# Kernel optimization log

Hardware: AMD Instinct MI355X
Metric: run time of the kernel (lower is better)

## Reference

```python
import jax, jax.numpy as jnp
import numpy as np

NX, NY = 2, 4          # Cpab tess_size [2, 4]
NT = 4 * NX * NY       # 4 triangles per cell = 32
NSTEPS = 50            # libcpab default numeric integration steps


def _build_tess():
    corner, verts = {}, []
    for j in range(NY + 1):
        for i in range(NX + 1):
            corner[(i, j)] = len(verts); verts.append((i / NX, j / NY))
    center = {}
    for j in range(NY):
        for i in range(NX):
            center[(i, j)] = len(verts); verts.append(((i + 0.5) / NX, (j + 0.5) / NY))
    verts = np.array(verts, np.float64)
    # zero_boundary=True: only interior grid corners + cell centers carry free velocity
    free = [corner[(i, j)] for j in range(1, NY) for i in range(1, NX)]
    free += [center[(i, j)] for j in range(NY) for i in range(NX)]
    tri_vidx = np.zeros((NT, 3), np.int32)
    invP = np.zeros((NT, 3, 3), np.float64)
    for j in range(NY):
        for i in range(NX):
            ll, lr = corner[(i, j)], corner[(i + 1, j)]
            ur, ul = corner[(i + 1, j + 1)], corner[(i, j + 1)]
            c = center[(i, j)]
            for k, tv in enumerate([(ll, lr, c), (lr, ur, c), (ur, ul, c), (ul, ll, c)]):
                t = 4 * (i + j * NX) + k
                tri_vidx[t] = tv
                P = np.vstack([verts[list(tv)].T, np.ones(3)])  # columns [p; 1]
                invP[t] = np.linalg.inv(P)
    return np.array(free, np.int32), tri_vidx, invP.astype(np.float32), len(verts)

FREE_IDX, TRI_VIDX, INVP, NV = _build_tess()
THETA_DIM = 2 * len(FREE_IDX)  # 22


def _findcell(p):
    # p: (..., 2) in [0,1]^2 -> flat triangle index in [0, NT)
    x = jnp.clip(p[..., 0], 0.0, 1.0) * NX
    y = jnp.clip(p[..., 1], 0.0, 1.0) * NY
    cx = jnp.clip(jnp.floor(x), 0, NX - 1)
    cy = jnp.clip(jnp.floor(y), 0, NY - 1)
    xr, yr = x - cx, y - cy
    below_diag = yr <= xr
    below_anti = yr <= 1.0 - xr
    tri = jnp.where(below_diag, jnp.where(below_anti, 0, 1),
                    jnp.where(below_anti, 3, 2))
    return (4 * (cx + cy * NX)).astype(jnp.int32) + tri


def _cpab_transform_grid(theta, H, W):
    # theta (B, 22) -> per-triangle affine maps A (B, NT, 2, 3), then Euler-integrate
    B = theta.shape[0]
    vv = jnp.zeros((B, NV, 2), theta.dtype).at[:, FREE_IDX].set(theta.reshape(B, -1, 2))
    V = vv[:, TRI_VIDX]                                            # (B,NT,3,2) vertex velocities
    A = jnp.einsum('btvc,tvw->btcw', V, jnp.asarray(INVP, theta.dtype))  # (B,NT,2,3)
    gx, gy = jnp.meshgrid(jnp.linspace(0.0, 1.0, W), jnp.linspace(0.0, 1.0, H))
    p0 = jnp.broadcast_to(jnp.stack([gx.ravel(), gy.ravel()], -1), (B, H * W, 2))
    dt = 1.0 / NSTEPS
    bidx = jnp.arange(B)[:, None]

    def step(p, _):
        Ai = A[bidx, _findcell(p)]                                 # (B,HW,2,3)
        v = Ai[..., 0] * p[..., :1] + Ai[..., 1] * p[..., 1:2] + Ai[..., 2]
        return p + dt * v, None

    p, _ = jax.lax.scan(step, p0, None, length=NSTEPS)
    return p                                                       # (B,HW,2)


def _bilinear(data, grid, H, W):
    # data (B,C,H,W), grid (B,HW,2) in [0,1]; clamp-to-border bilinear sampling
    B, C = data.shape[0], data.shape[1]
    gx = jnp.clip(grid[..., 0], 0.0, 1.0) * (W - 1)
    gy = jnp.clip(grid[..., 1], 0.0, 1.0) * (H - 1)
    x0 = jnp.clip(jnp.floor(gx).astype(jnp.int32), 0, W - 2)
    y0 = jnp.clip(jnp.floor(gy).astype(jnp.int32), 0, H - 2)
    wx, wy = gx - x0, gy - y0
    df = data.reshape(B, C, H * W)
    take = jax.vmap(lambda d, l: d[:, l])                          # per-batch gather

    def g(ix, iy):
        return take(df, iy * W + ix)                               # (B,C,HW)

    wx_, wy_ = wx[:, None, :], wy[:, None, :]
    out = (g(x0, y0) * (1 - wx_) * (1 - wy_)
           + g(x0 + 1, y0) * wx_ * (1 - wy_)
           + g(x0, y0 + 1) * (1 - wx_) * wy_
           + g(x0 + 1, y0 + 1) * wx_ * wy_)
    return out.reshape(B, C, H, W)


def setup_inputs() -> dict:
    key = jax.random.key(0)
    k1, k2 = jax.random.split(key)
    x = jax.random.normal(k1, (8, 256, 256, 64), dtype=jnp.float32)
    theta = jax.random.normal(k2, (8, THETA_DIM), dtype=jnp.float32)
    return {"x": x, "theta": theta}


def reference(x, theta):
    B, H, W, C = x.shape
    data = jnp.transpose(x, (0, 3, 1, 2))          # NHWC -> NCHW
    grid_t = _cpab_transform_grid(theta, H, W)     # integrate CPA velocity field
    out = _bilinear(data, grid_t, H, W)            # warp via bilinear sampling
    return jnp.transpose(out, (0, 2, 3, 1))        # NCHW -> NHWC
```

## Files before the change

kernel.cpp:

```cpp
#include <hip/hip_runtime.h>

#define NBATCH 8
#define HH 256
#define WW 256
#define CC 64
#define HWPTS 65536
#define NSTEPS_ 50

typedef float vf4 __attribute__((ext_vector_type(4)));

__global__ __launch_bounds__(256) void cpab_build_A(const float* __restrict__ theta,
                                                    float* __restrict__ Aout) {
  int tid = threadIdx.x;
  int b = tid >> 5, t = tid & 31;
  int cell = t >> 2, k = t & 3;
  int ci = cell & 1, cj = cell >> 1;
  int ll = cj * 3 + ci;
  int lr = ll + 1, ul = ll + 3, ur = ll + 4;
  int cen = 15 + cj * 2 + ci;
  int v0, v1, v2 = cen;
  if (k == 0)      { v0 = ll; v1 = lr; }
  else if (k == 1) { v0 = lr; v1 = ur; }
  else if (k == 2) { v0 = ur; v1 = ul; }
  else             { v0 = ul; v1 = ll; }

  int vs[3] = {v0, v1, v2};
  double xs[3], ys[3];
  float Vx[3], Vy[3];
  for (int q = 0; q < 3; ++q) {
    int v = vs[q];
    if (v < 15) { xs[q] = (double)(v % 3) * 0.5; ys[q] = (double)(v / 3) * 0.25; }
    else { int u = v - 15; xs[q] = ((double)(u & 1) + 0.5) * 0.5;
           ys[q] = ((double)(u >> 1) + 0.5) * 0.25; }
    int s = (v == 4) ? 0 : (v == 7) ? 1 : (v == 10) ? 2 : (v >= 15) ? (v - 12) : -1;
    if (s >= 0) { Vx[q] = theta[b * 22 + 2 * s]; Vy[q] = theta[b * 22 + 2 * s + 1]; }
    else        { Vx[q] = 0.f; Vy[q] = 0.f; }
  }
  double x0 = xs[0], x1 = xs[1], x2 = xs[2];
  double y0 = ys[0], y1 = ys[1], y2 = ys[2];
  double det = x0 * (y1 - y2) - x1 * (y0 - y2) + x2 * (y0 - y1);
  double inv[3][3] = {
      {y1 - y2, x2 - x1, x1 * y2 - x2 * y1},
      {y2 - y0, x0 - x2, x2 * y0 - x0 * y2},
      {y0 - y1, x1 - x0, x0 * y1 - x1 * y0}};
  for (int w = 0; w < 3; ++w) {
    float i0 = (float)(inv[0][w] / det);
    float i1 = (float)(inv[1][w] / det);
    float i2 = (float)(inv[2][w] / det);
    float ax = __fadd_rn(__fadd_rn(__fmul_rn(Vx[0], i0), __fmul_rn(Vx[1], i1)),
                         __fmul_rn(Vx[2], i2));
    float ay = __fadd_rn(__fadd_rn(__fmul_rn(Vy[0], i0), __fmul_rn(Vy[1], i1)),
                         __fmul_rn(Vy[2], i2));
    Aout[b * 192 + (w * 32 + t) * 2]     = ax;
    Aout[b * 192 + (w * 32 + t) * 2 + 1] = ay;
  }
}

__global__ __launch_bounds__(256, 8) void cpab_warp_sample(const float* __restrict__ xin,
                                                           const float* __restrict__ Ain,
                                                           float* __restrict__ out) {
  __shared__ float2 sA2[96];
  __shared__ int    sOff[256];
  __shared__ float4 sW[256];

  int tid = threadIdx.x;
  int bid = blockIdx.x;
  int b = bid & 7;
  int row = bid >> 3;
  int base_hw = row << 8;

  if (tid < 192) ((float*)sA2)[tid] = Ain[b * 192 + tid];
  __syncthreads();

  {
    float px = (tid == 255) ? 1.0f : __fmul_rn((float)tid, 1.0f / 255.0f);
    float py = (row == 255) ? 1.0f : __fmul_rn((float)row, 1.0f / 255.0f);
#pragma unroll 1
    for (int s = 0; s < NSTEPS_; ++s) {
      float xc = fminf(fmaxf(px, 0.f), 1.f) * 2.0f;
      float yc = fminf(fmaxf(py, 0.f), 1.f) * 4.0f;
      float cxf = fminf(floorf(xc), 1.0f);
      float cyf = fminf(floorf(yc), 3.0f);
      float xr = xc - cxf, yr = yc - cyf;
      int tri = (yr <= xr) ? ((yr <= 1.0f - xr) ? 0 : 1)
                           : ((yr <= 1.0f - xr) ? 3 : 2);
      int cid = ((((int)cyf) << 1) + (int)cxf) * 4 + tri;
      float2 q0 = sA2[cid];
      float2 q1 = sA2[32 + cid];
      float2 q2 = sA2[64 + cid];
      float vx = __fadd_rn(__fadd_rn(__fmul_rn(q0.x, px), __fmul_rn(q1.x, py)), q2.x);
      float vy = __fadd_rn(__fadd_rn(__fmul_rn(q0.y, px), __fmul_rn(q1.y, py)), q2.y);
      px = __fadd_rn(px, __fmul_rn(0.02f, vx));
      py = __fadd_rn(py, __fmul_rn(0.02f, vy));
    }
    float gx = __fmul_rn(fminf(fmaxf(px, 0.f), 1.f), 255.0f);
    float gy = __fmul_rn(fminf(fmaxf(py, 0.f), 1.f), 255.0f);
    int ix = min((int)gx, 254);
    int iy = min((int)gy, 254);
    float wx = __fadd_rn(gx, -(float)ix);
    float wy = __fadd_rn(gy, -(float)iy);
    sOff[tid] = (iy << 8) + ix;
    float4 w4;
    w4.x = (1.f - wx) * (1.f - wy);
    w4.y = wx * (1.f - wy);
    w4.z = (1.f - wx) * wy;
    w4.w = wx * wy;
    sW[tid] = w4;
  }

  int wv = tid >> 6;
  int lp = (tid >> 4) & 3;
  int lc = tid & 15;
  const float4* xb4 = (const float4*)(xin + (size_t)b * ((size_t)HWPTS * CC));
  float* ob = out + ((size_t)b * HWPTS + base_hw + (wv << 6)) * CC;

#pragma unroll
  for (int i = 0; i < 16; ++i) {
    int p = (wv << 6) + (i << 2) + lp;
    int off = sOff[p];
    float4 W = sW[p];
    const float4* q = xb4 + ((size_t)off << 4) + lc;
    float4 L0 = q[0];
    float4 L1 = q[16];
    float4 L2 = q[16 * 256];
    float4 L3 = q[16 * 256 + 16];
    vf4 o;
    o.x = L0.x * W.x + L1.x * W.y + L2.x * W.z + L3.x * W.w;
    o.y = L0.y * W.x + L1.y * W.y + L2.y * W.z + L3.y * W.w;
    o.z = L0.z * W.x + L1.z * W.y + L2.z * W.z + L3.z * W.w;
    o.w = L0.w * W.x + L1.w * W.y + L2.w * W.z + L3.w * W.w;
    __builtin_nontemporal_store(o, (vf4*)(ob + (size_t)((i << 2) + lp) * CC + (lc << 2)));
  }
}

extern "C" void kernel_launch(void* const* d_in, const int* in_sizes, int n_in,
                              void* d_out, int out_size, void* d_ws, size_t ws_size,
                              hipStream_t stream) {
  const float* x     = (const float*)d_in[0];
  const float* theta = (const float*)d_in[1];
  float* out  = (float*)d_out;
  float* Abuf = (float*)d_ws;

  cpab_build_A<<<1, 256, 0, stream>>>(theta, Abuf);
  cpab_warp_sample<<<NBATCH * HWPTS / 256, 256, 0, stream>>>(x, Abuf, out);
}
```

Baseline: 51.17 us.

## Specialize one wavefront as integration producer, overlap with gather consumers via LDS flag

Moves the 50-step CPA integration onto a single wavefront, which computes 64 points at a time and publishes each chunk through a workgroup-scope release flag. The other wavefronts spin on that flag and start the bilinear gather and store as soon as their points are ready. Gather work is spread across all four wavefronts with an interleaved point assignment. This is meant to overlap the serial integration with memory traffic. In exchange the integration runs four times longer on one wavefront, and the spin-wait adds synchronisation overhead.

```diff
diff --git a/kernel.cpp b/kernel.cpp
--- a/kernel.cpp
+++ b/kernel.cpp
@@ -56,80 +56,106 @@
   }
 }
 
-__global__ __launch_bounds__(256, 8) void cpab_warp_sample(const float* __restrict__ xin,
-                                                           const float* __restrict__ Ain,
-                                                           float* __restrict__ out) {
+__global__ __launch_bounds__(256, 8) void cpab_pc(const float* __restrict__ xin,
+                                                  const float* __restrict__ Ain,
+                                                  float* __restrict__ out) {
   __shared__ float2 sA2[96];
   __shared__ int    sOff[256];
   __shared__ float4 sW[256];
+  __shared__ int    sFlag;
 
   int tid = threadIdx.x;
   int bid = blockIdx.x;
   int b = bid & 7;
   int row = bid >> 3;
-  int base_hw = row << 8;
 
+  if (tid == 0) sFlag = 0;
   if (tid < 192) ((float*)sA2)[tid] = Ain[b * 192 + tid];
   __syncthreads();
 
-  {
-    float px = (tid == 255) ? 1.0f : __fmul_rn((float)tid, 1.0f / 255.0f);
-    float py = (row == 255) ? 1.0f : __fmul_rn((float)row, 1.0f / 255.0f);
+  int wv = tid >> 6;
+  int lane = tid & 63;
+  int lp = lane >> 4;
+  int lc = lane & 15;
+  const float4* xb4 = (const float4*)(xin + (size_t)b * ((size_t)HWPTS * CC));
+  float* ob = out + ((size_t)b * HWPTS + ((size_t)row << 8)) * CC;
+  float py_row = (row == 255) ? 1.0f : __fmul_rn((float)row, 1.0f / 255.0f);
+
+  if (wv == 3) {
 #pragma unroll 1
-    for (int s = 0; s < NSTEPS_; ++s) {
-      float xc = fminf(fmaxf(px, 0.f), 1.f) * 2.0f;
-      float yc = fminf(fmaxf(py, 0.f), 1.f) * 4.0f;
-      float cxf = fminf(floorf(xc), 1.0f);
-      float cyf = fminf(floorf(yc), 3.0f);
-      float xr = xc - cxf, yr = yc - cyf;
-      int tri = (yr <= xr) ? ((yr <= 1.0f - xr) ? 0 : 1)
-                           : ((yr <= 1.0f - xr) ? 3 : 2);
-      int cid = ((((int)cyf) << 1) + (int)cxf) * 4 + tri;
-      float2 q0 = sA2[cid];
-      float2 q1 = sA2[32 + cid];
-      float2 q2 = sA2[64 + cid];
-      float vx = __fadd_rn(__fadd_rn(__fmul_rn(q0.x, px), __fmul_rn(q1.x, py)), q2.x);
-      float vy = __fadd_rn(__fadd_rn(__fmul_rn(q0.y, px), __fmul_rn(q1.y, py)), q2.y);
-      px = __fadd_rn(px, __fmul_rn(0.02f, vx));
-      py = __fadd_rn(py, __fmul_rn(0.02f, vy));
+    for (int c = 0; c < 4; ++c) {
+      int p = (c << 6) + lane;
+      float px = (p == 255) ? 1.0f : __fmul_rn((float)p, 1.0f / 255.0f);
+      float py = py_row;
+#pragma unroll 1
+      for (int s = 0; s < NSTEPS_; ++s) {
+        float xc = fminf(fmaxf(px, 0.f), 1.f) * 2.0f;
+        float yc = fminf(fmaxf(py, 0.f), 1.f) * 4.0f;
+        float cxf = fminf(floorf(xc), 1.0f);
+        float cyf = fminf(floorf(yc), 3.0f);
+        float xr = xc - cxf, yr = yc - cyf;
+        int tri = (yr <= xr) ? ((yr <= 1.0f - xr) ? 0 : 1)
+                             : ((yr <= 1.0f - xr) ? 3 : 2);
+        int cid = ((((int)cyf) << 1) + (int)cxf) * 4 + tri;
+        float2 q0 = sA2[cid];
+        float2 q1 = sA2[32 + cid];
+        float2 q2 = sA2[64 + cid];
+        float vx = __fadd_rn(__fadd_rn(__fmul_rn(q0.x, px), __fmul_rn(q1.x, py)), q2.x);
+        float vy = __fadd_rn(__fadd_rn(__fmul_rn(q0.y, px), __fmul_rn(q1.y, py)), q2.y);
+        px = __fadd_rn(px, __fmul_rn(0.02f, vx));
+        py = __fadd_rn(py, __fmul_rn(0.02f, vy));
+      }
+      float gx = __fmul_rn(fminf(fmaxf(px, 0.f), 1.f), 255.0f);
+      float gy = __fmul_rn(fminf(fmaxf(py, 0.f), 1.f), 255.0f);
+      int ix = min((int)gx, 254);
+      int iy = min((int)gy, 254);
+      float wx = __fadd_rn(gx, -(float)ix);
+      float wy = __fadd_rn(gy, -(float)iy);
+      sOff[p] = (iy << 8) + ix;
+      float4 w4;
+      w4.x = (1.f - wx) * (1.f - wy);
+      w4.y = wx * (1.f - wy);
+      w4.z = (1.f - wx) * wy;
+      w4.w = wx * wy;
+      sW[p] = w4;
+      __hip_atomic_store(&sFlag, c + 1, __ATOMIC_RELEASE, __HIP_MEMORY_SCOPE_WORKGROUP);
     }
-    float gx = __fmul_rn(fminf(fmaxf(px, 0.f), 1.f), 255.0f);
-    float gy = __fmul_rn(fminf(fmaxf(py, 0.f), 1.f), 255.0f);
-    int ix = min((int)gx, 254);
-    int iy = min((int)gy, 254);
-    float wx = __fadd_rn(gx, -(float)ix);
-    float wy = __fadd_rn(gy, -(float)iy);
-    sOff[tid] = (iy << 8) + ix;
-    float4 w4;
-    w4.x = (1.f - wx) * (1.f - wy);
-    w4.y = wx * (1.f - wy);
-    w4.z = (1.f - wx) * wy;
-    w4.w = wx * wy;
-    sW[tid] = w4;
   }
 
-  int wv = tid >> 6;
-  int lp = (tid >> 4) & 3;
-  int lc = tid & 15;
-  const float4* xb4 = (const float4*)(xin + (size_t)b * ((size_t)HWPTS * CC));
-  float* ob = out + ((size_t)b * HWPTS + base_hw + (wv << 6)) * CC;
-
-#pragma unroll
-  for (int i = 0; i < 16; ++i) {
-    int p = (wv << 6) + (i << 2) + lp;
-    int off = sOff[p];
-    float4 W = sW[p];
-    const float4* q = xb4 + ((size_t)off << 4) + lc;
-    float4 L0 = q[0];
-    float4 L1 = q[16];
-    float4 L2 = q[16 * 256];
-    float4 L3 = q[16 * 256 + 16];
-    vf4 o;
-    o.x = L0.x * W.x + L1.x * W.y + L2.x * W.z + L3.x * W.w;
-    o.y = L0.y * W.x + L1.y * W.y + L2.y * W.z + L3.y * W.w;
-    o.z = L0.z * W.x + L1.z * W.y + L2.z * W.z + L3.z * W.w;
-    o.w = L0.w * W.x + L1.w * W.y + L2.w * W.z + L3.w * W.w;
-    __builtin_nontemporal_store(o, (vf4*)(ob + (size_t)((i << 2) + lp) * CC + (lc << 2)));
+#pragma unroll 1
+  for (int k = 0; k < 16; k += 2) {
+    int g0 = (k << 2) | wv;
+    int g1 = g0 + 4;
+    if (wv < 3) {
+      int need = (g1 >> 4) + 1;
+      while (__hip_atomic_load(&sFlag, __ATOMIC_ACQUIRE, __HIP_MEMORY_SCOPE_WORKGROUP) < need)
+        __builtin_amdgcn_s_sleep(2);
+    }
+    int p0 = (g0 << 2) + lp;
+    int p1 = (g1 << 2) + lp;
+    int off0 = sOff[p0];  float4 W0 = sW[p0];
+    int off1 = sOff[p1];  float4 W1 = sW[p1];
+    const float4* q0 = xb4 + ((size_t)off0 << 4) + lc;
+    const float4* q1 = xb4 + ((size_t)off1 << 4) + lc;
+    float4 A0 = q0[0];
+    float4 A1 = q0[16];
+    float4 A2 = q0[16 * 256];
+    float4 A3 = q0[16 * 256 + 16];
+    float4 B0 = q1[0];
+    float4 B1 = q1[16];
+    float4 B2 = q1[16 * 256];
+    float4 B3 = q1[16 * 256 + 16];
+    vf4 o0, o1;
+    o0.x = A0.x * W0.x + A1.x * W0.y + A2.x * W0.z + A3.x * W0.w;
+    o0.y = A0.y * W0.x + A1.y * W0.y + A2.y * W0.z + A3.y * W0.w;
+    o0.z = A0.z * W0.x + A1.z * W0.y + A2.z * W0.z + A3.z * W0.w;
+    o0.w = A0.w * W0.x + A1.w * W0.y + A2.w * W0.z + A3.w * W0.w;
+    o1.x = B0.x * W1.x + B1.x * W1.y + B2.x * W1.z + B3.x * W1.w;
+    o1.y = B0.y * W1.x + B1.y * W1.y + B2.y * W1.z + B3.y * W1.w;
+    o1.z = B0.z * W1.x + B1.z * W1.y + B2.z * W1.z + B3.z * W1.w;
+    o1.w = B0.w * W1.x + B1.w * W1.y + B2.w * W1.z + B3.w * W1.w;
+    __builtin_nontemporal_store(o0, (vf4*)(ob + (size_t)p0 * CC + (lc << 2)));
+    __builtin_nontemporal_store(o1, (vf4*)(ob + (size_t)p1 * CC + (lc << 2)));
   }
 }
 
@@ -142,5 +168,5 @@
   float* Abuf = (float*)d_ws;
 
   cpab_build_A<<<1, 256, 0, stream>>>(theta, Abuf);
-  cpab_warp_sample<<<NBATCH * HWPTS / 256, 256, 0, stream>>>(x, Abuf, out);
+  cpab_pc<<<NBATCH * HWPTS / 256, 256, 0, stream>>>(x, Abuf, out);
 }
```

Measured after the change: 50.49 us. Within noise of the previous version (-1.3%).
